# Kernel tuning notes

Measured on AMD Instinct MI355X. Metric: run time of the kernel, lower is better.

The kernel has to match this reference:

```python
import jax, jax.numpy as jnp
import numpy as np

B, T, D, H = 8, 4096, 512, 512


def log_g(x):
    # log of g(x) where g(x) = relu(x) + 0.5 for x >= 0, sigmoid(x) for x < 0
    return jnp.where(x >= 0, jnp.log(jax.nn.relu(x) + 0.5), -jax.nn.softplus(-x))


def setup_inputs() -> dict:
    key = jax.random.key(0)
    kx, kh0, kwz, kbz, kwh, kbh = jax.random.split(key, 6)
    s = 1.0 / np.sqrt(D)
    return {
        "x": jax.random.normal(kx, (B, T, D), dtype=jnp.float32),
        "h_0": jax.random.uniform(kh0, (B, H), dtype=jnp.float32),
        "Wz": jax.random.uniform(kwz, (H, D), dtype=jnp.float32, minval=-s, maxval=s),
        "bz": jax.random.uniform(kbz, (H,), dtype=jnp.float32, minval=-s, maxval=s),
        "Wh": jax.random.uniform(kwh, (H, D), dtype=jnp.float32, minval=-s, maxval=s),
        "bh": jax.random.uniform(kbh, (H,), dtype=jnp.float32, minval=-s, maxval=s),
    }


def parallel_scan_log(log_coeffs, log_values):
    # log_coeffs: (B, T, H), log_values: (B, T+1, H)
    a_star = jnp.cumsum(jnp.pad(log_coeffs, ((0, 0), (1, 0), (0, 0))), axis=1)  # (B, T+1, H)
    log_h = a_star + jax.lax.cumlogsumexp(log_values - a_star, axis=1)
    return jnp.exp(log_h)  # (B, T+1, H)


def reference(x, h_0, Wz, bz, Wh, bh):
    k = jnp.einsum('btd,hd->bth', x, Wz) + bz                # (B, T, H)
    log_z = -jax.nn.softplus(-k)                              # log sigmoid(k)
    log_coeffs = -jax.nn.softplus(k)                          # log (1 - sigmoid(k))
    log_h0 = log_g(h_0)[:, None, :]                           # (B, 1, H)
    log_tilde_h = log_g(jnp.einsum('btd,hd->bth', x, Wh) + bh)
    vals = jnp.concatenate([log_h0, log_z + log_tilde_h], axis=1)  # (B, T+1, H)
    h = parallel_scan_log(log_coeffs, vals)
    return h[:, -x.shape[1]:, :]                              # (B, T, H)
```

## Files before the change

kernel.cpp:

```cpp
#include <hip/hip_runtime.h>
#include <math.h>

#define Bq 8
#define Tq 4096
#define Dq 512
#define Hq 512
#define Mq (Bq * Tq)
#define NC 64
#define CL 64

typedef unsigned short ushort_t;
typedef unsigned int uint_t;
typedef __bf16 bf16x8 __attribute__((ext_vector_type(8)));
typedef float f32x4 __attribute__((ext_vector_type(4)));

__device__ __forceinline__ ushort_t f2bf(float f) {
    unsigned int u = __float_as_uint(f);
    unsigned int r = u + 0x7fffu + ((u >> 16) & 1u);
    return (ushort_t)(r >> 16);
}

__device__ __forceinline__ void gload16(const void* g, void* l) {
    __builtin_amdgcn_global_load_lds(
        (const __attribute__((address_space(1))) void*)g,
        (__attribute__((address_space(3))) void*)l, 16, 0, 0);
}

__device__ __forceinline__ void gates(uint_t w, float& c, float& v) {
    float k  = __uint_as_float((w & 0xffffu) << 16);
    float th = __uint_as_float(w & 0xffff0000u);
    float ek = __expf(k);
    c = 1.0f / (1.0f + ek);
    float z = 1.0f - c;
    float g = (th >= 0.0f) ? (th + 0.5f) : (1.0f / (1.0f + __expf(-th)));
    v = z * g;
}

__global__ __launch_bounds__(256)
void convert_w(const float* __restrict__ Wz, const float* __restrict__ Wh,
               ushort_t* __restrict__ dst) {
    size_t i8 = ((size_t)blockIdx.x * 256 + threadIdx.x) * 8;
    const size_t WN = (size_t)Hq * Dq;
    const float* src = (i8 < WN) ? Wz : Wh;
    size_t off = (i8 < WN) ? i8 : i8 - WN;
    float4 a = *reinterpret_cast<const float4*>(src + off);
    float4 b = *reinterpret_cast<const float4*>(src + off + 4);
    uint4 o;
    o.x = (uint_t)f2bf(a.x) | ((uint_t)f2bf(a.y) << 16);
    o.y = (uint_t)f2bf(a.z) | ((uint_t)f2bf(a.w) << 16);
    o.z = (uint_t)f2bf(b.x) | ((uint_t)f2bf(b.y) << 16);
    o.w = (uint_t)f2bf(b.z) | ((uint_t)f2bf(b.w) << 16);
    *reinterpret_cast<uint4*>(dst + i8) = o;
}

__global__ __launch_bounds__(256, 2)
void gemm_fused(const float* __restrict__ x, const ushort_t* __restrict__ wb,
                const float* __restrict__ bz, const float* __restrict__ bh,
                uint_t* __restrict__ kvout, float2* __restrict__ chAW) {
    __shared__ __align__(16) ushort_t smem[3 * 128 * 64];
    ushort_t* As  = smem;
    ushort_t* Bzs = smem + 128 * 64;
    ushort_t* Bhs = smem + 2 * 128 * 64;

    const int tid  = threadIdx.x;
    const int lane = tid & 63;
    const int wave = tid >> 6;
    const int wm = (wave >> 1) * 64;
    const int wn = (wave & 1) * 64;
    const int mBase = blockIdx.x * 128;
    const int nBase = blockIdx.y * 128;
    const ushort_t* Wzb = wb;
    const ushort_t* Whb = wb + (size_t)Hq * Dq;

    f32x4 zero = {0.f, 0.f, 0.f, 0.f};
    f32x4 accz[4][4], acch[4][4];
#pragma unroll
    for (int i = 0; i < 4; ++i)
#pragma unroll
        for (int j = 0; j < 4; ++j) { accz[i][j] = zero; acch[i][j] = zero; }

    const int rowInW = lane >> 3;
    const int ccG = (lane & 7) ^ rowInW;
    const int swz = lane & 7;

    for (int k0 = 0; k0 < Dq; k0 += 64) {
#pragma unroll
        for (int j = 0; j < 4; ++j) {
            const int rseg = j * 4 + wave;
            const int row  = rseg * 8 + rowInW;
            const size_t gcol = (size_t)(k0 + ccG * 8);
            const float* xs = x + (size_t)(mBase + row) * Dq + gcol;
            float4 a = *reinterpret_cast<const float4*>(xs);
            float4 b = *reinterpret_cast<const float4*>(xs + 4);
            uint4 o;
            o.x = (uint_t)f2bf(a.x) | ((uint_t)f2bf(a.y) << 16);
            o.y = (uint_t)f2bf(a.z) | ((uint_t)f2bf(a.w) << 16);
            o.z = (uint_t)f2bf(b.x) | ((uint_t)f2bf(b.y) << 16);
            o.w = (uint_t)f2bf(b.z) | ((uint_t)f2bf(b.w) << 16);
            *reinterpret_cast<uint4*>(As + rseg * 512 + lane * 8) = o;
            gload16(Wzb + (size_t)(nBase + row) * Dq + gcol, &Bzs[rseg * 512]);
            gload16(Whb + (size_t)(nBase + row) * Dq + gcol, &Bhs[rseg * 512]);
        }
        __syncthreads();

#pragma unroll
        for (int ks = 0; ks < 2; ++ks) {
            const int cc = ks * 4 + (lane >> 4);
            const int sc = cc ^ swz;
            bf16x8 af[4], bzf[4], bhf[4];
#pragma unroll
            for (int i = 0; i < 4; ++i) {
                int rowA = wm + i * 16 + (lane & 15);
                af[i] = *reinterpret_cast<const bf16x8*>(&As[rowA * 64 + sc * 8]);
            }
#pragma unroll
            for (int i = 0; i < 4; ++i) {
                int rowB = wn + i * 16 + (lane & 15);
                bzf[i] = *reinterpret_cast<const bf16x8*>(&Bzs[rowB * 64 + sc * 8]);
                bhf[i] = *reinterpret_cast<const bf16x8*>(&Bhs[rowB * 64 + sc * 8]);
            }
#pragma unroll
            for (int mi = 0; mi < 4; ++mi)
#pragma unroll
                for (int ni = 0; ni < 4; ++ni) {
                    accz[mi][ni] = __builtin_amdgcn_mfma_f32_16x16x32_bf16(
                        af[mi], bzf[ni], accz[mi][ni], 0, 0, 0);
                    acch[mi][ni] = __builtin_amdgcn_mfma_f32_16x16x32_bf16(
                        af[mi], bhf[ni], acch[mi][ni], 0, 0, 0);
                }
        }
        __syncthreads();
    }

    const int colL = lane & 15;
    const int quad = lane >> 4;
    float2* sb = reinterpret_cast<float2*>(smem) + wave * 1024;

#pragma unroll
    for (int ni = 0; ni < 4; ++ni) {
        int h = nBase + wn + ni * 16 + colL;
        float bzv = bz[h];
        float bhv = bh[h];
#pragma unroll
        for (int mi = 0; mi < 4; ++mi) {
            float A = 1.f, W = 0.f;
#pragma unroll
            for (int r = 0; r < 4; ++r) {
                int bt = mBase + wm + mi * 16 + quad * 4 + r;
                float kf  = accz[mi][ni][r] + bzv;
                float thf = acch[mi][ni][r] + bhv;
                uint_t word = (uint_t)f2bf(kf) | ((uint_t)f2bf(thf) << 16);
                kvout[(size_t)bt * Hq + h] = word;
                float c, v;
                gates(word, c, v);
                W = fmaf(c, W, v);
                A *= c;
            }
            sb[(mi * 4 + quad) * 64 + ni * 16 + colL] = make_float2(A, W);
        }
    }
    __syncthreads();
    {
        float A = 1.f, W = 0.f;
#pragma unroll
        for (int s = 0; s < 16; ++s) {
            float2 aw = sb[s * 64 + lane];
            W = fmaf(aw.x, W, aw.y);
            A *= aw.x;
        }
        int g = blockIdx.x * 2 + (wm >> 6);
        int h = nBase + wn + lane;
        chAW[(size_t)g * Hq + h] = make_float2(A, W);
    }
}

__global__ __launch_bounds__(512)
void scan_final(const uint_t* kv, const float* __restrict__ h0,
                const float2* __restrict__ chAW, float* out) {
    const int b = blockIdx.x & 7;
    const int chunk = 63 - (blockIdx.x >> 3);
    const int h = threadIdx.x;

    float x0 = h0[(size_t)b * Hq + h];
    float r = (x0 >= 0.f) ? (x0 + 0.5f) : (1.f / (1.f + __expf(-x0)));

    const float2* p = chAW + (size_t)b * NC * Hq + h;
    int j = 0;
    for (; j + 8 <= chunk; j += 8) {
        float2 aw[8];
#pragma unroll
        for (int q = 0; q < 8; ++q) aw[q] = p[(size_t)(j + q) * Hq];
#pragma unroll
        for (int q = 0; q < 8; ++q) r = fmaf(aw[q].x, r, aw[q].y);
    }
    for (; j < chunk; ++j) {
        float2 aw = p[(size_t)j * Hq];
        r = fmaf(aw.x, r, aw.y);
    }

    const size_t base = ((size_t)b * Tq + (size_t)chunk * CL) * Hq + h;
    const uint_t* kvp = kv + base;
    float* op = out + base;

    uint_t w[16];
#pragma unroll
    for (int q = 0; q < 16; ++q) w[q] = kvp[(size_t)q * Hq];
    for (int bt = 0; bt < 4; ++bt) {
        uint_t wn[16];
        if (bt < 3) {
#pragma unroll
            for (int q = 0; q < 16; ++q)
                wn[q] = kvp[(size_t)((bt + 1) * 16 + q) * Hq];
        }
#pragma unroll
        for (int q = 0; q < 16; ++q) {
            float c, v;
            gates(w[q], c, v);
            r = fmaf(c, r, v);
            op[(size_t)(bt * 16 + q) * Hq] = r;
        }
#pragma unroll
        for (int q = 0; q < 16; ++q) w[q] = wn[q];
    }
}

extern "C" void kernel_launch(void* const* d_in, const int* in_sizes, int n_in,
                              void* d_out, int out_size, void* d_ws, size_t ws_size,
                              hipStream_t stream) {
    const float* x  = (const float*)d_in[0];
    const float* h0 = (const float*)d_in[1];
    const float* Wz = (const float*)d_in[2];
    const float* bz = (const float*)d_in[3];
    const float* Wh = (const float*)d_in[4];
    const float* bh = (const float*)d_in[5];
    float* out = (float*)d_out;

    char* ws = (char*)d_ws;
    ushort_t* wb = (ushort_t*)ws;
    float2* chAW = (float2*)(wb + 2 * (size_t)Hq * Dq);
    uint_t* kv = (uint_t*)d_out;

    const int wConv = (2 * Hq * Dq) / (256 * 8);
    convert_w<<<dim3(wConv), dim3(256), 0, stream>>>(Wz, Wh, wb);
    gemm_fused<<<dim3(Mq / 128, Hq / 128), dim3(256), 0, stream>>>(x, wb, bz, bh, kv, chAW);
    scan_final<<<dim3(Bq * NC), dim3(512), 0, stream>>>(kv, h0, chAW, out);
}
```

Before: 195.1 us.

## Interleave Wz/Wh into one weight matrix and halve per-block GEMM tile

Packs Wz and Wh into a single interleaved bf16 weight matrix in 16-row groups so each GEMM block computes both gates for 64 hidden units with one accumulator set. This halves accumulator registers and LDS so occupancy can rise to three blocks per CU. A 1D grid with a remapped block order replaces the 2D grid. In exchange, the grid doubles, so the fp32 x tiles are read and converted to bf16 twice as often.

```diff
diff --git a/kernel.cpp b/kernel.cpp
--- a/kernel.cpp
+++ b/kernel.cpp
@@ -8,6 +8,7 @@
 #define Mq (Bq * Tq)
 #define NC 64
 #define CL 64
+#define NP 1024
 
 typedef unsigned short ushort_t;
 typedef unsigned int uint_t;
@@ -40,11 +41,13 @@
 void convert_w(const float* __restrict__ Wz, const float* __restrict__ Wh,
                ushort_t* __restrict__ dst) {
     size_t i8 = ((size_t)blockIdx.x * 256 + threadIdx.x) * 8;
-    const size_t WN = (size_t)Hq * Dq;
-    const float* src = (i8 < WN) ? Wz : Wh;
-    size_t off = (i8 < WN) ? i8 : i8 - WN;
-    float4 a = *reinterpret_cast<const float4*>(src + off);
-    float4 b = *reinterpret_cast<const float4*>(src + off + 4);
+    int np = (int)(i8 >> 9);
+    int d0 = (int)(i8 & (Dq - 1));
+    int h  = ((np >> 5) << 4) | (np & 15);
+    const float* src = ((np >> 4) & 1) ? Wh : Wz;
+    src += (size_t)h * Dq + d0;
+    float4 a = *reinterpret_cast<const float4*>(src);
+    float4 b = *reinterpret_cast<const float4*>(src + 4);
     uint4 o;
     o.x = (uint_t)f2bf(a.x) | ((uint_t)f2bf(a.y) << 16);
     o.y = (uint_t)f2bf(a.z) | ((uint_t)f2bf(a.w) << 16);
@@ -53,31 +56,30 @@
     *reinterpret_cast<uint4*>(dst + i8) = o;
 }
 
-__global__ __launch_bounds__(256, 2)
+__global__ __launch_bounds__(256, 3)
 void gemm_fused(const float* __restrict__ x, const ushort_t* __restrict__ wb,
                 const float* __restrict__ bz, const float* __restrict__ bh,
                 uint_t* __restrict__ kvout, float2* __restrict__ chAW) {
-    __shared__ __align__(16) ushort_t smem[3 * 128 * 64];
-    ushort_t* As  = smem;
-    ushort_t* Bzs = smem + 128 * 64;
-    ushort_t* Bhs = smem + 2 * 128 * 64;
+    __shared__ __align__(16) ushort_t smem[2 * 128 * 64];
+    ushort_t* As = smem;
+    ushort_t* Bs = smem + 128 * 64;
+
+    const int logical = (blockIdx.x & 7) * 256 + (blockIdx.x >> 3);
+    const int mBase = (logical >> 3) * 128;
+    const int nBase = (logical & 7) * 128;
 
     const int tid  = threadIdx.x;
     const int lane = tid & 63;
     const int wave = tid >> 6;
     const int wm = (wave >> 1) * 64;
     const int wn = (wave & 1) * 64;
-    const int mBase = blockIdx.x * 128;
-    const int nBase = blockIdx.y * 128;
-    const ushort_t* Wzb = wb;
-    const ushort_t* Whb = wb + (size_t)Hq * Dq;
 
     f32x4 zero = {0.f, 0.f, 0.f, 0.f};
-    f32x4 accz[4][4], acch[4][4];
+    f32x4 acc[4][4];
 #pragma unroll
     for (int i = 0; i < 4; ++i)
 #pragma unroll
-        for (int j = 0; j < 4; ++j) { accz[i][j] = zero; acch[i][j] = zero; }
+        for (int j = 0; j < 4; ++j) acc[i][j] = zero;
 
     const int rowInW = lane >> 3;
     const int ccG = (lane & 7) ^ rowInW;
@@ -89,6 +91,7 @@
             const int rseg = j * 4 + wave;
             const int row  = rseg * 8 + rowInW;
             const size_t gcol = (size_t)(k0 + ccG * 8);
+            gload16(wb + (size_t)(nBase + row) * Dq + gcol, &Bs[rseg * 512]);
             const float* xs = x + (size_t)(mBase + row) * Dq + gcol;
             float4 a = *reinterpret_cast<const float4*>(xs);
             float4 b = *reinterpret_cast<const float4*>(xs + 4);
@@ -98,8 +101,6 @@
             o.z = (uint_t)f2bf(b.x) | ((uint_t)f2bf(b.y) << 16);
             o.w = (uint_t)f2bf(b.z) | ((uint_t)f2bf(b.w) << 16);
             *reinterpret_cast<uint4*>(As + rseg * 512 + lane * 8) = o;
-            gload16(Wzb + (size_t)(nBase + row) * Dq + gcol, &Bzs[rseg * 512]);
-            gload16(Whb + (size_t)(nBase + row) * Dq + gcol, &Bhs[rseg * 512]);
         }
         __syncthreads();
 
@@ -107,38 +108,32 @@
         for (int ks = 0; ks < 2; ++ks) {
             const int cc = ks * 4 + (lane >> 4);
             const int sc = cc ^ swz;
-            bf16x8 af[4], bzf[4], bhf[4];
+            bf16x8 af[4], bf[4];
 #pragma unroll
             for (int i = 0; i < 4; ++i) {
                 int rowA = wm + i * 16 + (lane & 15);
                 af[i] = *reinterpret_cast<const bf16x8*>(&As[rowA * 64 + sc * 8]);
+                int rowB = wn + i * 16 + (lane & 15);
+                bf[i] = *reinterpret_cast<const bf16x8*>(&Bs[rowB * 64 + sc * 8]);
             }
 #pragma unroll
-            for (int i = 0; i < 4; ++i) {
-                int rowB = wn + i * 16 + (lane & 15);
-                bzf[i] = *reinterpret_cast<const bf16x8*>(&Bzs[rowB * 64 + sc * 8]);
-                bhf[i] = *reinterpret_cast<const bf16x8*>(&Bhs[rowB * 64 + sc * 8]);
-            }
-#pragma unroll
             for (int mi = 0; mi < 4; ++mi)
 #pragma unroll
-                for (int ni = 0; ni < 4; ++ni) {
-                    accz[mi][ni] = __builtin_amdgcn_mfma_f32_16x16x32_bf16(
-                        af[mi], bzf[ni], accz[mi][ni], 0, 0, 0);
-                    acch[mi][ni] = __builtin_amdgcn_mfma_f32_16x16x32_bf16(
-                        af[mi], bhf[ni], acch[mi][ni], 0, 0, 0);
-                }
+                for (int ni = 0; ni < 4; ++ni)
+                    acc[mi][ni] = __builtin_amdgcn_mfma_f32_16x16x32_bf16(
+                        af[mi], bf[ni], acc[mi][ni], 0, 0, 0);
         }
         __syncthreads();
     }
 
     const int colL = lane & 15;
     const int quad = lane >> 4;
-    float2* sb = reinterpret_cast<float2*>(smem) + wave * 1024;
-
-#pragma unroll
-    for (int ni = 0; ni < 4; ++ni) {
-        int h = nBase + wn + ni * 16 + colL;
+    const int hOff = (nBase >> 1) + ((wave & 1) << 5);
+    float2* sb = reinterpret_cast<float2*>(smem) + wave * 512;
+
+#pragma unroll
+    for (int q = 0; q < 2; ++q) {
+        int h = hOff + q * 16 + colL;
         float bzv = bz[h];
         float bhv = bh[h];
 #pragma unroll
@@ -147,8 +142,8 @@
 #pragma unroll
             for (int r = 0; r < 4; ++r) {
                 int bt = mBase + wm + mi * 16 + quad * 4 + r;
-                float kf  = accz[mi][ni][r] + bzv;
-                float thf = acch[mi][ni][r] + bhv;
+                float kf  = acc[mi][2 * q][r] + bzv;
+                float thf = acc[mi][2 * q + 1][r] + bhv;
                 uint_t word = (uint_t)f2bf(kf) | ((uint_t)f2bf(thf) << 16);
                 kvout[(size_t)bt * Hq + h] = word;
                 float c, v;
@@ -156,20 +151,20 @@
                 W = fmaf(c, W, v);
                 A *= c;
             }
-            sb[(mi * 4 + quad) * 64 + ni * 16 + colL] = make_float2(A, W);
+            sb[(mi * 4 + quad) * 32 + q * 16 + colL] = make_float2(A, W);
         }
     }
     __syncthreads();
-    {
+    if (lane < 32) {
         float A = 1.f, W = 0.f;
 #pragma unroll
         for (int s = 0; s < 16; ++s) {
-            float2 aw = sb[s * 64 + lane];
+            float2 aw = sb[s * 32 + lane];
             W = fmaf(aw.x, W, aw.y);
             A *= aw.x;
         }
-        int g = blockIdx.x * 2 + (wm >> 6);
-        int h = nBase + wn + lane;
+        int g = (mBase >> 6) + (wm >> 6);
+        int h = hOff + lane;
         chAW[(size_t)g * Hq + h] = make_float2(A, W);
     }
 }
@@ -237,11 +232,11 @@
 
     char* ws = (char*)d_ws;
     ushort_t* wb = (ushort_t*)ws;
-    float2* chAW = (float2*)(wb + 2 * (size_t)Hq * Dq);
+    float2* chAW = (float2*)(wb + (size_t)NP * Dq);
     uint_t* kv = (uint_t*)d_out;
 
-    const int wConv = (2 * Hq * Dq) / (256 * 8);
+    const int wConv = (NP * Dq) / (256 * 8);
     convert_w<<<dim3(wConv), dim3(256), 0, stream>>>(Wz, Wh, wb);
-    gemm_fused<<<dim3(Mq / 128, Hq / 128), dim3(256), 0, stream>>>(x, wb, bz, bh, kv, chAW);
+    gemm_fused<<<dim3((Mq / 128) * (NP / 128)), dim3(256), 0, stream>>>(x, wb, bz, bh, kv, chAW);
     scan_final<<<dim3(Bq * NC), dim3(512), 0, stream>>>(kv, h0, chAW, out);
 }
```

Measured after the change: 212.3 us. +8.8%, slower.
